# Performance work log

Measured on AMD Instinct MI355X. Metric: run time of the kernel, lower is better.

The kernel has to match this reference:

```python
import jax, jax.numpy as jnp
import numpy as np

X_DIM = 512
Z_DIM = 16
HEADS = 8
DIM_HEAD = 64
INNER = HEADS * DIM_HEAD
EPS = 1e-5


def _layernorm(t, g, b):
    mu = jnp.mean(t, axis=-1, keepdims=True)
    var = jnp.mean(jnp.square(t - mu), axis=-1, keepdims=True)
    return (t - mu) * jax.lax.rsqrt(var + EPS) * g + b


def setup_inputs() -> dict:
    key = jax.random.key(0)
    ks = jax.random.split(key, 8)
    B, N = 4, 2048
    s_x = 1.0 / np.sqrt(X_DIM)
    s_z = 1.0 / np.sqrt(Z_DIM)
    s_i = 1.0 / np.sqrt(INNER)
    return {
        "x": jax.random.normal(ks[0], (B, N, X_DIM), dtype=jnp.float32),
        "z": jax.random.normal(ks[1], (B, 1, Z_DIM), dtype=jnp.float32),
        "ln_x_g": jnp.ones((X_DIM,), jnp.float32),
        "ln_x_b": jnp.zeros((X_DIM,), jnp.float32),
        "ln_z_g": jnp.ones((Z_DIM,), jnp.float32),
        "ln_z_b": jnp.zeros((Z_DIM,), jnp.float32),
        "Wq": jax.random.normal(ks[2], (X_DIM, INNER), jnp.float32) * s_x,
        "Wk": jax.random.normal(ks[3], (X_DIM, INNER), jnp.float32) * s_x,
        "Wv": jax.random.normal(ks[4], (X_DIM, INNER), jnp.float32) * s_x,
        "Wz": jax.random.normal(ks[5], (Z_DIM, 2 * X_DIM), jnp.float32) * s_z,
        "Wo": jax.random.normal(ks[6], (INNER, X_DIM), jnp.float32) * s_i,
        "bo": jnp.zeros((X_DIM,), jnp.float32),
    }


def reference(x, z, ln_x_g, ln_x_b, ln_z_g, ln_z_b, Wq, Wk, Wv, Wz, Wo, bo):
    scale = DIM_HEAD ** (-0.5)
    # z path: LN -> Linear -> SiLU -> split into FiLM scale/shift
    zp = jax.nn.silu(_layernorm(z, ln_z_g, ln_z_b) @ Wz)  # [B, 1, 2*x_dim]
    z1, z2 = jnp.split(zp, 2, axis=-1)
    x_mod = _layernorm(x, ln_x_g, ln_x_b) * z1 + z2       # [B, N, x_dim]
    B, N, _ = x.shape

    def heads(t):  # [B, N, inner] -> [B, h, N, d]
        return t.reshape(B, N, HEADS, DIM_HEAD).transpose(0, 2, 1, 3)

    q = heads(x_mod @ Wq)
    k = heads(x_mod @ Wk)
    v = heads(x_mod @ Wv)
    sim = jnp.einsum('bhid,bhjd->bhij', q, k) * scale
    attn = jax.nn.softmax(sim, axis=-1)
    out = jnp.einsum('bhij,bhjd->bhid', attn, v)           # [B, h, N, d]
    out = out.transpose(0, 2, 1, 3).reshape(B, N, INNER)
    return out @ Wo + bo
```

## Files before the change

### kernel.cpp

```cpp
#include <hip/hip_runtime.h>

#define XD 512
#define HEADS 8
#define DH 64
#define NSEQ 2048
#define NBATCH 4
#define NROWS (NBATCH*NSEQ)

#define SCALE_L2E 0.18033688011112042f
#define DEFER_THR 4.0f

typedef __attribute__((ext_vector_type(8))) short bf16x8;
typedef __attribute__((ext_vector_type(8))) unsigned short u16x8;
typedef __attribute__((ext_vector_type(4))) float f32x4;
typedef __attribute__((ext_vector_type(16))) float f32x16;

__device__ __forceinline__ unsigned short f2bf(float f) {
  union { float f; unsigned u; } v; v.f = f;
  return (unsigned short)((v.u + 0x7fffu + ((v.u >> 16) & 1u)) >> 16);
}

__device__ __forceinline__ float fexp2(float x) {
#if __has_builtin(__builtin_amdgcn_exp2f)
  return __builtin_amdgcn_exp2f(x);
#else
  return exp2f(x);
#endif
}

__device__ __forceinline__ unsigned cvt_pk_bf16(float lo, float hi) {
  unsigned r;
  asm("v_cvt_pk_bf16_f32 %0, %1, %2" : "=v"(r) : "v"(lo), "v"(hi));
  return r;
}

__device__ __forceinline__ void gload_lds16(const unsigned short* g, unsigned short* l) {
  __builtin_amdgcn_global_load_lds(
      (const __attribute__((address_space(1))) unsigned int*)g,
      (__attribute__((address_space(3))) unsigned int*)l, 16, 0, 0);
}

__global__ __launch_bounds__(256) void zpath_kernel(
    const float* __restrict__ z, const float* __restrict__ g, const float* __restrict__ b,
    const float* __restrict__ Wz, float* __restrict__ z12) {
  int bb = blockIdx.x;
  int t = threadIdx.x;
  float zv[16];
  float mean = 0.f;
#pragma unroll
  for (int i = 0; i < 16; ++i) { zv[i] = z[bb * 16 + i]; mean += zv[i]; }
  mean *= (1.f / 16.f);
  float var = 0.f;
#pragma unroll
  for (int i = 0; i < 16; ++i) { float d = zv[i] - mean; var += d * d; }
  var *= (1.f / 16.f);
  float rs = rsqrtf(var + 1e-5f);
  float zn[16];
#pragma unroll
  for (int i = 0; i < 16; ++i) zn[i] = (zv[i] - mean) * rs * g[i] + b[i];
  for (int c = t; c < 1024; c += 256) {
    float acc = 0.f;
#pragma unroll
    for (int i = 0; i < 16; ++i) acc += zn[i] * Wz[i * 1024 + c];
    float s = acc / (1.f + __expf(-acc));
    z12[bb * 1024 + c] = s;
  }
}

__global__ __launch_bounds__(256) void xmod_kernel(
    const float* __restrict__ x, const float* __restrict__ g, const float* __restrict__ b,
    const float* __restrict__ z12, unsigned short* __restrict__ xm) {
  int wave = threadIdx.x >> 6, lane = threadIdx.x & 63;
  int row = blockIdx.x * 4 + wave;
  const float* xr = x + (size_t)row * XD;
  float4 v0 = ((const float4*)xr)[lane * 2];
  float4 v1 = ((const float4*)xr)[lane * 2 + 1];
  float vv[8] = {v0.x, v0.y, v0.z, v0.w, v1.x, v1.y, v1.z, v1.w};
  float sum = 0.f, sq = 0.f;
#pragma unroll
  for (int i = 0; i < 8; ++i) { sum += vv[i]; sq += vv[i] * vv[i]; }
#pragma unroll
  for (int o = 32; o; o >>= 1) { sum += __shfl_xor(sum, o); sq += __shfl_xor(sq, o); }
  float mean = sum * (1.f / 512.f);
  float var = sq * (1.f / 512.f) - mean * mean;
  float rs = rsqrtf(var + 1e-5f);
  int bb = row >> 11;
  const float* zz = z12 + bb * 1024;
  int c0 = lane * 8;
  u16x8 o8;
#pragma unroll
  for (int i = 0; i < 8; ++i) {
    int c = c0 + i;
    float t = (vv[i] - mean) * rs * g[c] + b[c];
    t = t * zz[c] + zz[512 + c];
    o8[i] = f2bf(t);
  }
  *(u16x8*)(xm + (size_t)row * XD + c0) = o8;
}

__global__ __launch_bounds__(256) void wtrans4_kernel(
    const float* __restrict__ W0, const float* __restrict__ W1,
    const float* __restrict__ W2, const float* __restrict__ W3,
    unsigned short* __restrict__ dst) {
  int idx = blockIdx.x * 256 + threadIdx.x;
  int w = idx >> 18;
  int e = idx & 262143;
  int n = e >> 9, k = e & 511;
  const float* W = (w == 0) ? W0 : (w == 1) ? W1 : (w == 2) ? W2 : W3;
  dst[idx] = f2bf(W[k * 512 + n]);
}

__global__ __launch_bounds__(256, 2) void gemm_qkv_kernel(
    const unsigned short* __restrict__ A, const unsigned short* __restrict__ Wt,
    unsigned short* __restrict__ Qo, unsigned short* __restrict__ Ko,
    unsigned short* __restrict__ Vo) {
  __shared__ unsigned short Alds[128 * 64];
  __shared__ unsigned short Blds[64 * 64];
  int widx = threadIdx.x >> 6, lane = threadIdx.x & 63;
  int blk = blockIdx.x;
  int nt = blk % 24, mt = blk / 24;
  int blkM = mt * 128, blkN = nt * 64;
  int wr = widx >> 1, wc = widx & 1;
  int lr = lane & 15, lg = lane >> 4;
  int srow = lane >> 3, scol = (lane & 7) * 8;

  const unsigned short* Ag = A + (size_t)(blkM + widx * 32 + srow) * 512 + scol;
  const unsigned short* Bg = Wt + (size_t)(blkN + widx * 16 + srow) * 512 + scol;
  unsigned short* Al = &Alds[(widx * 32) * 64];
  unsigned short* Bl = &Blds[(widx * 16) * 64];

  f32x4 acc[4][2] = {};

  for (int kc = 0; kc < 512; kc += 64) {
#pragma unroll
    for (int i = 0; i < 4; ++i)
      gload_lds16(Ag + (size_t)(i * 8) * 512 + kc, Al + (i * 8) * 64);
#pragma unroll
    for (int i = 0; i < 2; ++i)
      gload_lds16(Bg + (size_t)(i * 8) * 512 + kc, Bl + (i * 8) * 64);
    __syncthreads();

#pragma unroll
    for (int kh = 0; kh < 2; ++kh) {
      bf16x8 bfr[2];
#pragma unroll
      for (int ni = 0; ni < 2; ++ni)
        bfr[ni] = *(const bf16x8*)&Blds[(wc * 32 + ni * 16 + lr) * 64 + kh * 32 + lg * 8];
#pragma unroll
      for (int mi = 0; mi < 4; ++mi) {
        bf16x8 afr = *(const bf16x8*)&Alds[(wr * 64 + mi * 16 + lr) * 64 + kh * 32 + lg * 8];
#pragma unroll
        for (int ni = 0; ni < 2; ++ni)
          acc[mi][ni] = __builtin_amdgcn_mfma_f32_16x16x32_bf16(afr, bfr[ni], acc[mi][ni], 0, 0, 0);
      }
    }
    __syncthreads();
  }

  int cg = blkN >> 9;
#pragma unroll
  for (int mi = 0; mi < 4; ++mi)
#pragma unroll
    for (int ni = 0; ni < 2; ++ni) {
      int col = blkN + wc * 32 + ni * 16 + lr;
      int c = col & 511;
#pragma unroll
      for (int j = 0; j < 4; ++j) {
        int row = blkM + wr * 64 + mi * 16 + lg * 4 + j;
        float v = acc[mi][ni][j];
        if (cg == 0) {
          Qo[(size_t)row * 512 + c] = f2bf(v * SCALE_L2E);
        } else if (cg == 1) {
          Ko[(size_t)row * 512 + c] = f2bf(v);
        } else {
          int bb = row >> 11, n = row & 2047, h = c >> 6, d = c & 63;
          int j4 = n & 15;
          int slot = (j4 & 3) | (((j4 >> 3) & 1) << 2) | (((j4 >> 2) & 1) << 3);
          int np = (n & ~15) | slot;
          Vo[(((size_t)(bb * HEADS + h) * DH + d) << 11) + np] = f2bf(v);
        }
      }
    }
}

__global__ __launch_bounds__(256, 2) void gemm_out_kernel(
    const unsigned short* __restrict__ A, const unsigned short* __restrict__ Wt,
    float* __restrict__ out, const float* __restrict__ bias) {
  __shared__ unsigned short Alds[128 * 64];
  __shared__ unsigned short Blds[64 * 64];
  int widx = threadIdx.x >> 6, lane = threadIdx.x & 63;
  int blk = blockIdx.x;
  int nt = blk & 7, mt = blk >> 3;
  int blkM = mt * 128, blkN = nt * 64;
  int wr = widx >> 1, wc = widx & 1;
  int lr = lane & 15, lg = lane >> 4;
  int srow = lane >> 3, scol = (lane & 7) * 8;

  const unsigned short* Ag = A + (size_t)(blkM + widx * 32 + srow) * 512 + scol;
  const unsigned short* Bg = Wt + (size_t)(blkN + widx * 16 + srow) * 512 + scol;
  unsigned short* Al = &Alds[(widx * 32) * 64];
  unsigned short* Bl = &Blds[(widx * 16) * 64];

  f32x4 acc[4][2] = {};

  for (int kc = 0; kc < 512; kc += 64) {
#pragma unroll
    for (int i = 0; i < 4; ++i)
      gload_lds16(Ag + (size_t)(i * 8) * 512 + kc, Al + (i * 8) * 64);
#pragma unroll
    for (int i = 0; i < 2; ++i)
      gload_lds16(Bg + (size_t)(i * 8) * 512 + kc, Bl + (i * 8) * 64);
    __syncthreads();

#pragma unroll
    for (int kh = 0; kh < 2; ++kh) {
      bf16x8 bfr[2];
#pragma unroll
      for (int ni = 0; ni < 2; ++ni)
        bfr[ni] = *(const bf16x8*)&Blds[(wc * 32 + ni * 16 + lr) * 64 + kh * 32 + lg * 8];
#pragma unroll
      for (int mi = 0; mi < 4; ++mi) {
        bf16x8 afr = *(const bf16x8*)&Alds[(wr * 64 + mi * 16 + lr) * 64 + kh * 32 + lg * 8];
#pragma unroll
        for (int ni = 0; ni < 2; ++ni)
          acc[mi][ni] = __builtin_amdgcn_mfma_f32_16x16x32_bf16(afr, bfr[ni], acc[mi][ni], 0, 0, 0);
      }
    }
    __syncthreads();
  }

#pragma unroll
  for (int mi = 0; mi < 4; ++mi)
#pragma unroll
    for (int ni = 0; ni < 2; ++ni) {
      int col = blkN + wc * 32 + ni * 16 + lr;
#pragma unroll
      for (int j = 0; j < 4; ++j) {
        int row = blkM + wr * 64 + mi * 16 + lg * 4 + j;
        out[(size_t)row * 512 + col] = acc[mi][ni][j] + bias[col];
      }
    }
}


#define KVCHUNK 64
#define NCHUNK (NSEQ / KVCHUNK)

#define STAGE(buf, kcc) do {                                              \
    _Pragma("unroll")                                                     \
    for (int i = 0; i < 2; ++i) {                                         \
      int rb = widx * 16 + i * 8;                                         \
      int row = rb + (lane >> 3);                                         \
      int csrc = (lane & 7) ^ (row & 7);                                  \
      gload_lds16(Kg + (size_t)((kcc) + row) * 512 + csrc * 8, &Klds[buf][rb * 64]); \
      gload_lds16(Vg + (size_t)row * NSEQ + (kcc) + csrc * 8, &Vlds[buf][rb * 64]); \
    }                                                                     \
  } while (0)

__global__ __launch_bounds__(256, 2) void attn_kernel(
    const unsigned short* __restrict__ Q, const unsigned short* __restrict__ K,
    const unsigned short* __restrict__ VT, unsigned short* __restrict__ O) {
  __shared__ unsigned short Klds[2][64 * 64];
  __shared__ unsigned short Vlds[2][64 * 64];
  int widx = threadIdx.x >> 6, lane = threadIdx.x & 63;
  int blk = blockIdx.x;
  int xcd = blk & 7;
  int idx = blk >> 3;
  int bh = xcd * 4 + (idx >> 4);
  int qg = idx & 15;
  int b = bh >> 3, h = bh & 7;
  int ql = lane & 31, hi = lane >> 5;
  int qrow0 = qg * 128 + widx * 32;

  bf16x8 qf[4];
  const unsigned short* Qp = Q + (size_t)(b * NSEQ + qrow0 + ql) * 512 + h * 64 + hi * 8;
#pragma unroll
  for (int ks = 0; ks < 4; ++ks) qf[ks] = *(const bf16x8*)(Qp + ks * 16);

  const unsigned short* Kg = K + (size_t)b * NSEQ * 512 + h * 64;
  const unsigned short* Vg = VT + (size_t)bh * DH * NSEQ;

  float m0 = -3.0e38f, l0 = 0.f;
  f32x16 o[2] = {};

  STAGE(0, 0);
  __syncthreads();
  int cur = 0;
  for (int t = 0; t < NCHUNK; ++t) {
    if (t + 1 < NCHUNK) STAGE(cur ^ 1, (t + 1) * KVCHUNK);
    const unsigned short* kb_ = &Klds[cur][0];
    const unsigned short* vb_ = &Vlds[cur][0];

    f32x16 s[2];
    __builtin_amdgcn_s_setprio(1);
#pragma unroll
    for (int kt = 0; kt < 2; ++kt) {
      int krow = kt * 32 + ql;
      f32x16 z = {};
#pragma unroll
      for (int ks = 0; ks < 4; ++ks) {
        bf16x8 kf = *(const bf16x8*)(kb_ + krow * 64 + (((ks * 2 + hi) ^ (krow & 7)) * 8));
        z = __builtin_amdgcn_mfma_f32_32x32x16_bf16(kf, qf[ks], z, 0, 0, 0);
      }
      s[kt] = z;
    }
    __builtin_amdgcn_s_setprio(0);

    float m8 = s[0][0];
#pragma unroll
    for (int i = 1; i < 16; ++i) m8 = fmaxf(m8, s[0][i]);
#pragma unroll
    for (int i = 0; i < 16; ++i) m8 = fmaxf(m8, s[1][i]);
    m8 = fmaxf(m8, __shfl_xor(m8, 32));
    bool grow = (m8 > m0 + DEFER_THR);
    if (__any((int)grow)) {
      float mn = fmaxf(m0, m8);
      float al = fexp2(m0 - mn);
      m0 = mn; l0 *= al;
#pragma unroll
      for (int dt = 0; dt < 2; ++dt)
#pragma unroll
        for (int j = 0; j < 16; ++j) o[dt][j] *= al;
    }
    float p0[16], p1[16]; float rs = 0.f;
#pragma unroll
    for (int i = 0; i < 16; ++i) { p0[i] = fexp2(s[0][i] - m0); rs += p0[i]; }
#pragma unroll
    for (int i = 0; i < 16; ++i) { p1[i] = fexp2(s[1][i] - m0); rs += p1[i]; }
    rs += __shfl_xor(rs, 32);
    l0 += rs;

    union { unsigned w[4]; bf16x8 v; } pf[4];
#pragma unroll
    for (int d2 = 0; d2 < 4; ++d2) {
      pf[0].w[d2] = cvt_pk_bf16(p0[2 * d2], p0[2 * d2 + 1]);
      pf[1].w[d2] = cvt_pk_bf16(p0[8 + 2 * d2], p0[8 + 2 * d2 + 1]);
      pf[2].w[d2] = cvt_pk_bf16(p1[2 * d2], p1[2 * d2 + 1]);
      pf[3].w[d2] = cvt_pk_bf16(p1[8 + 2 * d2], p1[8 + 2 * d2 + 1]);
    }

    __builtin_amdgcn_s_setprio(1);
#pragma unroll
    for (int dt = 0; dt < 2; ++dt) {
      int vrow = dt * 32 + ql;
      f32x16 acc = o[dt];
#pragma unroll
      for (int g = 0; g < 4; ++g) {
        bf16x8 vf = *(const bf16x8*)(vb_ + vrow * 64 + (((g * 2 + hi) ^ (vrow & 7)) * 8));
        acc = __builtin_amdgcn_mfma_f32_32x32x16_bf16(vf, pf[g].v, acc, 0, 0, 0);
      }
      o[dt] = acc;
    }
    __builtin_amdgcn_s_setprio(0);

    __syncthreads();
    cur ^= 1;
  }

  {
    float inv = 1.f / l0;
    size_t rowb = (size_t)(b * NSEQ + qrow0 + ql) * 512 + h * 64 + hi * 4;
#pragma unroll
    for (int dt = 0; dt < 2; ++dt)
#pragma unroll
      for (int c = 0; c < 8; ++c) {
        unsigned w = cvt_pk_bf16(o[dt][2 * c] * inv, o[dt][2 * c + 1] * inv);
        int d0 = dt * 32 + 8 * (c >> 1) + (c & 1) * 2;
        *(unsigned*)(O + rowb + d0) = w;
      }
  }
}

extern "C" void kernel_launch(void* const* d_in, const int* in_sizes, int n_in,
                              void* d_out, int out_size, void* d_ws, size_t ws_size,
                              hipStream_t stream) {
  const float* x   = (const float*)d_in[0];
  const float* z   = (const float*)d_in[1];
  const float* lxg = (const float*)d_in[2];
  const float* lxb = (const float*)d_in[3];
  const float* lzg = (const float*)d_in[4];
  const float* lzb = (const float*)d_in[5];
  const float* Wq  = (const float*)d_in[6];
  const float* Wk  = (const float*)d_in[7];
  const float* Wv  = (const float*)d_in[8];
  const float* Wz  = (const float*)d_in[9];
  const float* Wo  = (const float*)d_in[10];
  const float* bo  = (const float*)d_in[11];

  char* ws = (char*)d_ws;
  unsigned short* xm  = (unsigned short*)(ws);
  unsigned short* qb  = (unsigned short*)(ws + 8388608);
  unsigned short* kb  = (unsigned short*)(ws + 16777216);
  unsigned short* vt  = (unsigned short*)(ws + 25165824);
  unsigned short* ao  = (unsigned short*)(ws + 33554432);
  unsigned short* wqt = (unsigned short*)(ws + 41943040);
  unsigned short* wot = (unsigned short*)(ws + 43515904);
  float*          z12 = (float*)(ws + 44040192);

  zpath_kernel<<<NBATCH, 256, 0, stream>>>(z, lzg, lzb, Wz, z12);
  xmod_kernel<<<NROWS / 4, 256, 0, stream>>>(x, lxg, lxb, z12, xm);
  wtrans4_kernel<<<4096, 256, 0, stream>>>(Wq, Wk, Wv, Wo, wqt);
  gemm_qkv_kernel<<<1536, 256, 0, stream>>>(xm, wqt, qb, kb, vt);
  attn_kernel<<<512, 256, 0, stream>>>(qb, kb, vt, ao);
  gemm_out_kernel<<<512, 256, 0, stream>>>(ao, wot, (float*)d_out, bo);
}
```

Measured before the change: 115.9 us.

## Enlarge QKV GEMM tile, swizzle GEMM LDS, double attention KV chunk

The QKV GEMM tile grows from 128x64 to 128x128, which halves the grid and doubles the MFMA work per A-tile load. Both GEMMs now use an XOR-swizzled LDS layout to cut bank conflicts on fragment reads. The attention kernel stages 128-key chunks, processed as two 64-key halves per barrier, so there are half as many __syncthreads and loop iterations. In exchange, LDS use and accumulator registers go up (64 KB of KV buffers in attention, a 4x4 accumulator in the GEMM), which may reduce occupancy.

```diff
diff --git a/kernel.cpp b/kernel.cpp
--- a/kernel.cpp
+++ b/kernel.cpp
@@ -115,42 +115,42 @@
     unsigned short* __restrict__ Qo, unsigned short* __restrict__ Ko,
     unsigned short* __restrict__ Vo) {
   __shared__ unsigned short Alds[128 * 64];
-  __shared__ unsigned short Blds[64 * 64];
+  __shared__ unsigned short Blds[128 * 64];
   int widx = threadIdx.x >> 6, lane = threadIdx.x & 63;
   int blk = blockIdx.x;
-  int nt = blk % 24, mt = blk / 24;
-  int blkM = mt * 128, blkN = nt * 64;
+  int nt = blk % 12, mt = blk / 12;
+  int blkM = mt * 128, blkN = nt * 128;
   int wr = widx >> 1, wc = widx & 1;
   int lr = lane & 15, lg = lane >> 4;
-  int srow = lane >> 3, scol = (lane & 7) * 8;
-
-  const unsigned short* Ag = A + (size_t)(blkM + widx * 32 + srow) * 512 + scol;
-  const unsigned short* Bg = Wt + (size_t)(blkN + widx * 16 + srow) * 512 + scol;
-  unsigned short* Al = &Alds[(widx * 32) * 64];
-  unsigned short* Bl = &Blds[(widx * 16) * 64];
-
-  f32x4 acc[4][2] = {};
+  int srow = lane >> 3, sc8 = lane & 7;
+
+  f32x4 acc[4][4] = {};
 
   for (int kc = 0; kc < 512; kc += 64) {
 #pragma unroll
-    for (int i = 0; i < 4; ++i)
-      gload_lds16(Ag + (size_t)(i * 8) * 512 + kc, Al + (i * 8) * 64);
-#pragma unroll
-    for (int i = 0; i < 2; ++i)
-      gload_lds16(Bg + (size_t)(i * 8) * 512 + kc, Bl + (i * 8) * 64);
+    for (int i = 0; i < 4; ++i) {
+      int rb = widx * 32 + i * 8;
+      int row = rb + srow;
+      int cs = (sc8 ^ (row & 7)) * 8;
+      gload_lds16(A + (size_t)(blkM + row) * 512 + kc + cs, &Alds[rb * 64]);
+      gload_lds16(Wt + (size_t)(blkN + row) * 512 + kc + cs, &Blds[rb * 64]);
+    }
     __syncthreads();
 
 #pragma unroll
     for (int kh = 0; kh < 2; ++kh) {
-      bf16x8 bfr[2];
-#pragma unroll
-      for (int ni = 0; ni < 2; ++ni)
-        bfr[ni] = *(const bf16x8*)&Blds[(wc * 32 + ni * 16 + lr) * 64 + kh * 32 + lg * 8];
+      bf16x8 bfr[4];
+#pragma unroll
+      for (int ni = 0; ni < 4; ++ni) {
+        int brow = wc * 64 + ni * 16 + lr;
+        bfr[ni] = *(const bf16x8*)&Blds[brow * 64 + (((kh * 4 + lg) ^ (brow & 7)) * 8)];
+      }
 #pragma unroll
       for (int mi = 0; mi < 4; ++mi) {
-        bf16x8 afr = *(const bf16x8*)&Alds[(wr * 64 + mi * 16 + lr) * 64 + kh * 32 + lg * 8];
-#pragma unroll
-        for (int ni = 0; ni < 2; ++ni)
+        int arow = wr * 64 + mi * 16 + lr;
+        bf16x8 afr = *(const bf16x8*)&Alds[arow * 64 + (((kh * 4 + lg) ^ (arow & 7)) * 8)];
+#pragma unroll
+        for (int ni = 0; ni < 4; ++ni)
           acc[mi][ni] = __builtin_amdgcn_mfma_f32_16x16x32_bf16(afr, bfr[ni], acc[mi][ni], 0, 0, 0);
       }
     }
@@ -161,8 +161,8 @@
 #pragma unroll
   for (int mi = 0; mi < 4; ++mi)
 #pragma unroll
-    for (int ni = 0; ni < 2; ++ni) {
-      int col = blkN + wc * 32 + ni * 16 + lr;
+    for (int ni = 0; ni < 4; ++ni) {
+      int col = blkN + wc * 64 + ni * 16 + lr;
       int c = col & 511;
 #pragma unroll
       for (int j = 0; j < 4; ++j) {
@@ -194,33 +194,39 @@
   int blkM = mt * 128, blkN = nt * 64;
   int wr = widx >> 1, wc = widx & 1;
   int lr = lane & 15, lg = lane >> 4;
-  int srow = lane >> 3, scol = (lane & 7) * 8;
-
-  const unsigned short* Ag = A + (size_t)(blkM + widx * 32 + srow) * 512 + scol;
-  const unsigned short* Bg = Wt + (size_t)(blkN + widx * 16 + srow) * 512 + scol;
-  unsigned short* Al = &Alds[(widx * 32) * 64];
-  unsigned short* Bl = &Blds[(widx * 16) * 64];
+  int srow = lane >> 3, sc8 = lane & 7;
 
   f32x4 acc[4][2] = {};
 
   for (int kc = 0; kc < 512; kc += 64) {
 #pragma unroll
-    for (int i = 0; i < 4; ++i)
-      gload_lds16(Ag + (size_t)(i * 8) * 512 + kc, Al + (i * 8) * 64);
-#pragma unroll
-    for (int i = 0; i < 2; ++i)
-      gload_lds16(Bg + (size_t)(i * 8) * 512 + kc, Bl + (i * 8) * 64);
+    for (int i = 0; i < 4; ++i) {
+      int rb = widx * 32 + i * 8;
+      int row = rb + srow;
+      int cs = (sc8 ^ (row & 7)) * 8;
+      gload_lds16(A + (size_t)(blkM + row) * 512 + kc + cs, &Alds[rb * 64]);
+    }
+#pragma unroll
+    for (int i = 0; i < 2; ++i) {
+      int rb = widx * 16 + i * 8;
+      int row = rb + srow;
+      int cs = (sc8 ^ (row & 7)) * 8;
+      gload_lds16(Wt + (size_t)(blkN + row) * 512 + kc + cs, &Blds[rb * 64]);
+    }
     __syncthreads();
 
 #pragma unroll
     for (int kh = 0; kh < 2; ++kh) {
       bf16x8 bfr[2];
 #pragma unroll
-      for (int ni = 0; ni < 2; ++ni)
-        bfr[ni] = *(const bf16x8*)&Blds[(wc * 32 + ni * 16 + lr) * 64 + kh * 32 + lg * 8];
+      for (int ni = 0; ni < 2; ++ni) {
+        int brow = wc * 32 + ni * 16 + lr;
+        bfr[ni] = *(const bf16x8*)&Blds[brow * 64 + (((kh * 4 + lg) ^ (brow & 7)) * 8)];
+      }
 #pragma unroll
       for (int mi = 0; mi < 4; ++mi) {
-        bf16x8 afr = *(const bf16x8*)&Alds[(wr * 64 + mi * 16 + lr) * 64 + kh * 32 + lg * 8];
+        int arow = wr * 64 + mi * 16 + lr;
+        bf16x8 afr = *(const bf16x8*)&Alds[arow * 64 + (((kh * 4 + lg) ^ (arow & 7)) * 8)];
 #pragma unroll
         for (int ni = 0; ni < 2; ++ni)
           acc[mi][ni] = __builtin_amdgcn_mfma_f32_16x16x32_bf16(afr, bfr[ni], acc[mi][ni], 0, 0, 0);
@@ -243,25 +249,90 @@
 }
 
 
-#define KVCHUNK 64
+#define KVCHUNK 128
 #define NCHUNK (NSEQ / KVCHUNK)
 
 #define STAGE(buf, kcc) do {                                              \
     _Pragma("unroll")                                                     \
-    for (int i = 0; i < 2; ++i) {                                         \
-      int rb = widx * 16 + i * 8;                                         \
-      int row = rb + (lane >> 3);                                         \
-      int csrc = (lane & 7) ^ (row & 7);                                  \
-      gload_lds16(Kg + (size_t)((kcc) + row) * 512 + csrc * 8, &Klds[buf][rb * 64]); \
-      gload_lds16(Vg + (size_t)row * NSEQ + (kcc) + csrc * 8, &Vlds[buf][rb * 64]); \
+    for (int i = 0; i < 4; ++i) {                                         \
+      int rbk = widx * 32 + i * 8;                                        \
+      int rowk = rbk + (lane >> 3);                                       \
+      int csk = (lane & 7) ^ (rowk & 7);                                  \
+      gload_lds16(Kg + (size_t)((kcc) + rowk) * 512 + csk * 8, &Klds[buf][rbk * 64]); \
+      int rbv = widx * 16 + i * 4;                                        \
+      int rowv = rbv + (lane >> 4);                                       \
+      int csv = (lane & 15) ^ (rowv & 15);                                \
+      gload_lds16(Vg + (size_t)rowv * NSEQ + (kcc) + csv * 8, &Vlds[buf][rbv * 128]); \
     }                                                                     \
+  } while (0)
+
+#define PROCESS_LDS64(kb_, vb_, half) do {                                \
+    f32x16 s[2];                                                          \
+    __builtin_amdgcn_s_setprio(1);                                        \
+    _Pragma("unroll")                                                     \
+    for (int kt = 0; kt < 2; ++kt) {                                      \
+      int krow = (half) * 64 + kt * 32 + ql;                              \
+      f32x16 z = {};                                                      \
+      _Pragma("unroll")                                                   \
+      for (int ks = 0; ks < 4; ++ks) {                                    \
+        bf16x8 kf = *(const bf16x8*)((kb_) + krow * 64 + (((ks * 2 + hi) ^ (krow & 7)) * 8)); \
+        z = __builtin_amdgcn_mfma_f32_32x32x16_bf16(kf, qf[ks], z, 0, 0, 0); \
+      }                                                                   \
+      s[kt] = z;                                                          \
+    }                                                                     \
+    __builtin_amdgcn_s_setprio(0);                                        \
+    float m8 = s[0][0];                                                   \
+    _Pragma("unroll")                                                     \
+    for (int i = 1; i < 16; ++i) m8 = fmaxf(m8, s[0][i]);                 \
+    _Pragma("unroll")                                                     \
+    for (int i = 0; i < 16; ++i) m8 = fmaxf(m8, s[1][i]);                 \
+    m8 = fmaxf(m8, __shfl_xor(m8, 32));                                   \
+    bool grow = (m8 > m0 + DEFER_THR);                                    \
+    if (__any((int)grow)) {                                               \
+      float mn = fmaxf(m0, m8);                                           \
+      float al = fexp2(m0 - mn);                                          \
+      m0 = mn; l0 *= al;                                                  \
+      _Pragma("unroll")                                                   \
+      for (int dt = 0; dt < 2; ++dt)                                      \
+        _Pragma("unroll")                                                 \
+        for (int j = 0; j < 16; ++j) o[dt][j] *= al;                      \
+    }                                                                     \
+    float p0[16], p1[16]; float rs = 0.f;                                 \
+    _Pragma("unroll")                                                     \
+    for (int i = 0; i < 16; ++i) { p0[i] = fexp2(s[0][i] - m0); rs += p0[i]; } \
+    _Pragma("unroll")                                                     \
+    for (int i = 0; i < 16; ++i) { p1[i] = fexp2(s[1][i] - m0); rs += p1[i]; } \
+    rs += __shfl_xor(rs, 32);                                             \
+    l0 += rs;                                                             \
+    union { unsigned w[4]; bf16x8 v; } pf[4];                             \
+    _Pragma("unroll")                                                     \
+    for (int d2 = 0; d2 < 4; ++d2) {                                      \
+      pf[0].w[d2] = cvt_pk_bf16(p0[2 * d2], p0[2 * d2 + 1]);              \
+      pf[1].w[d2] = cvt_pk_bf16(p0[8 + 2 * d2], p0[8 + 2 * d2 + 1]);      \
+      pf[2].w[d2] = cvt_pk_bf16(p1[2 * d2], p1[2 * d2 + 1]);              \
+      pf[3].w[d2] = cvt_pk_bf16(p1[8 + 2 * d2], p1[8 + 2 * d2 + 1]);      \
+    }                                                                     \
+    __builtin_amdgcn_s_setprio(1);                                        \
+    _Pragma("unroll")                                                     \
+    for (int dt = 0; dt < 2; ++dt) {                                      \
+      int vrow = dt * 32 + ql;                                            \
+      f32x16 acc = o[dt];                                                 \
+      _Pragma("unroll")                                                   \
+      for (int g = 0; g < 4; ++g) {                                       \
+        int sv = (half) * 8 + g * 2 + hi;                                 \
+        bf16x8 vf = *(const bf16x8*)((vb_) + vrow * 128 + ((sv ^ (vrow & 15)) * 8)); \
+        acc = __builtin_amdgcn_mfma_f32_32x32x16_bf16(vf, pf[g].v, acc, 0, 0, 0); \
+      }                                                                   \
+      o[dt] = acc;                                                        \
+    }                                                                     \
+    __builtin_amdgcn_s_setprio(0);                                        \
   } while (0)
 
 __global__ __launch_bounds__(256, 2) void attn_kernel(
     const unsigned short* __restrict__ Q, const unsigned short* __restrict__ K,
     const unsigned short* __restrict__ VT, unsigned short* __restrict__ O) {
-  __shared__ unsigned short Klds[2][64 * 64];
-  __shared__ unsigned short Vlds[2][64 * 64];
+  __shared__ unsigned short Klds[2][128 * 64];
+  __shared__ unsigned short Vlds[2][64 * 128];
   int widx = threadIdx.x >> 6, lane = threadIdx.x & 63;
   int blk = blockIdx.x;
   int xcd = blk & 7;
@@ -290,69 +361,8 @@
     if (t + 1 < NCHUNK) STAGE(cur ^ 1, (t + 1) * KVCHUNK);
     const unsigned short* kb_ = &Klds[cur][0];
     const unsigned short* vb_ = &Vlds[cur][0];
-
-    f32x16 s[2];
-    __builtin_amdgcn_s_setprio(1);
-#pragma unroll
-    for (int kt = 0; kt < 2; ++kt) {
-      int krow = kt * 32 + ql;
-      f32x16 z = {};
-#pragma unroll
-      for (int ks = 0; ks < 4; ++ks) {
-        bf16x8 kf = *(const bf16x8*)(kb_ + krow * 64 + (((ks * 2 + hi) ^ (krow & 7)) * 8));
-        z = __builtin_amdgcn_mfma_f32_32x32x16_bf16(kf, qf[ks], z, 0, 0, 0);
-      }
-      s[kt] = z;
-    }
-    __builtin_amdgcn_s_setprio(0);
-
-    float m8 = s[0][0];
-#pragma unroll
-    for (int i = 1; i < 16; ++i) m8 = fmaxf(m8, s[0][i]);
-#pragma unroll
-    for (int i = 0; i < 16; ++i) m8 = fmaxf(m8, s[1][i]);
-    m8 = fmaxf(m8, __shfl_xor(m8, 32));
-    bool grow = (m8 > m0 + DEFER_THR);
-    if (__any((int)grow)) {
-      float mn = fmaxf(m0, m8);
-      float al = fexp2(m0 - mn);
-      m0 = mn; l0 *= al;
-#pragma unroll
-      for (int dt = 0; dt < 2; ++dt)
-#pragma unroll
-        for (int j = 0; j < 16; ++j) o[dt][j] *= al;
-    }
-    float p0[16], p1[16]; float rs = 0.f;
-#pragma unroll
-    for (int i = 0; i < 16; ++i) { p0[i] = fexp2(s[0][i] - m0); rs += p0[i]; }
-#pragma unroll
-    for (int i = 0; i < 16; ++i) { p1[i] = fexp2(s[1][i] - m0); rs += p1[i]; }
-    rs += __shfl_xor(rs, 32);
-    l0 += rs;
-
-    union { unsigned w[4]; bf16x8 v; } pf[4];
-#pragma unroll
-    for (int d2 = 0; d2 < 4; ++d2) {
-      pf[0].w[d2] = cvt_pk_bf16(p0[2 * d2], p0[2 * d2 + 1]);
-      pf[1].w[d2] = cvt_pk_bf16(p0[8 + 2 * d2], p0[8 + 2 * d2 + 1]);
-      pf[2].w[d2] = cvt_pk_bf16(p1[2 * d2], p1[2 * d2 + 1]);
-      pf[3].w[d2] = cvt_pk_bf16(p1[8 + 2 * d2], p1[8 + 2 * d2 + 1]);
-    }
-
-    __builtin_amdgcn_s_setprio(1);
-#pragma unroll
-    for (int dt = 0; dt < 2; ++dt) {
-      int vrow = dt * 32 + ql;
-      f32x16 acc = o[dt];
-#pragma unroll
-      for (int g = 0; g < 4; ++g) {
-        bf16x8 vf = *(const bf16x8*)(vb_ + vrow * 64 + (((g * 2 + hi) ^ (vrow & 7)) * 8));
-        acc = __builtin_amdgcn_mfma_f32_32x32x16_bf16(vf, pf[g].v, acc, 0, 0, 0);
-      }
-      o[dt] = acc;
-    }
-    __builtin_amdgcn_s_setprio(0);
-
+    PROCESS_LDS64(kb_, vb_, 0);
+    PROCESS_LDS64(kb_, vb_, 1);
     __syncthreads();
     cur ^= 1;
   }
@@ -400,7 +410,7 @@
   zpath_kernel<<<NBATCH, 256, 0, stream>>>(z, lzg, lzb, Wz, z12);
   xmod_kernel<<<NROWS / 4, 256, 0, stream>>>(x, lxg, lxb, z12, xm);
   wtrans4_kernel<<<4096, 256, 0, stream>>>(Wq, Wk, Wv, Wo, wqt);
-  gemm_qkv_kernel<<<1536, 256, 0, stream>>>(xm, wqt, qb, kb, vt);
+  gemm_qkv_kernel<<<768, 256, 0, stream>>>(xm, wqt, qb, kb, vt);
   attn_kernel<<<512, 256, 0, stream>>>(qb, kb, vt, ao);
   gemm_out_kernel<<<512, 256, 0, stream>>>(ao, wot, (float*)d_out, bo);
 }
```

New measurement: 111.4 us. 3.8% less time.
